# Optimization experiments

Measured on AMD Instinct MI355X. Metric: run time of the kernel, lower is better.

## Reference

```python
import jax, jax.numpy as jnp
import numpy as np

# init_kwargs constants
MIN_T = 0.01
MAX_T = 0.5
TGT_MIN = 0.005
TGT_MAX = 0.03
W_MIN = 15.0
W_MAX = 5.0
W_CONT = 5.0
W_SIZE = 7.0
LESION_T = 0.3


def setup_inputs() -> dict:
    key = jax.random.key(0)
    pred = jax.random.uniform(key, (16, 1, 128, 128, 128), dtype=jnp.float32)
    return {"pred": pred}


def reference(pred):
    # pred: [B, 1, D, H, W]
    s = pred[:, 0]  # [B, D, H, W]
    B = s.shape[0]
    axes = (1, 2, 3)

    # -- min/max activation penalties (per-sample threshold means) --
    act = jnp.mean((s > MIN_T).astype(s.dtype), axis=axes)          # [B]
    loss = jax.nn.relu(TGT_MIN - act) * W_MIN
    high = jnp.mean((s > MAX_T).astype(s.dtype), axis=axes)
    loss = loss + jax.nn.relu(high - TGT_MAX) * W_MAX

    # -- continuity penalty: mean abs finite differences along D,H,W --
    d_grad = jnp.mean(jnp.abs(s[:, 1:] - s[:, :-1]), axis=axes)
    h_grad = jnp.mean(jnp.abs(s[:, :, 1:] - s[:, :, :-1]), axis=axes)
    w_grad = jnp.mean(jnp.abs(s[:, :, :, 1:] - s[:, :, :, :-1]), axis=axes)
    avg_grad = (d_grad + h_grad + w_grad) / 3.0
    has_lesion = jnp.any(s > LESION_T, axis=axes)
    loss = loss + jnp.where(has_lesion, jnp.minimum(avg_grad, 1.0), 0.0) * W_CONT

    # -- size-variance penalty over masked active values (unbiased std, torch.std) --
    mask = (s > MIN_T).astype(s.dtype)
    cnt = jnp.sum(mask, axis=axes)                                   # [B]
    cnt_safe = jnp.maximum(cnt, 1.0)
    m = jnp.sum(s * mask, axis=axes) / cnt_safe                      # masked mean [B]
    sq = jnp.sum(mask * (s - m[:, None, None, None]) ** 2, axis=axes)
    gate = (act > 0.001) & (cnt > 1.0)
    var = jnp.where(gate, sq / jnp.maximum(cnt - 1.0, 1.0), 1.0)     # guard sqrt/grad when gated off
    std = jnp.sqrt(var)
    rel_std = std / (m + 1e-6)
    pen = jnp.exp(-5.0 * rel_std)
    loss = loss + jnp.where(gate, pen, 0.0) * W_SIZE

    return jnp.sum(loss) / B
```

## Files before the change

kernel.cpp:

```cpp
#include <hip/hip_runtime.h>
#include <math.h>

#define MIN_T    0.01f
#define MAX_T    0.5f
#define LESION_T 0.3f

constexpr int NB       = 16;
constexpr int DIM      = 128;
constexpr int PLANE_F4 = DIM * DIM / 4;
constexpr int VOX      = DIM * DIM * DIM;
constexpr int THREADS  = 256;
constexpr int HWBLKS   = PLANE_F4 / THREADS;
constexpr int DSEGS    = 4;
constexpr int DPS      = DIM / DSEGS;
constexpr int NACC     = 8;

__global__ __launch_bounds__(THREADS)
void partial_kernel(const float* __restrict__ pred, double* __restrict__ acc)
{
    const int seg   = blockIdx.x;
    const int hwblk = blockIdx.y;
    const int b     = blockIdx.z;
    const int tid   = (int)threadIdx.x;

    const float4* __restrict__ s4 =
        reinterpret_cast<const float4*>(pred + (size_t)b * VOX);

    const int  h    = hwblk * 8 + (tid >> 5);
    const bool do_h = (h < DIM - 1);
    const bool do_w = ((tid & 31) != 31);

    const int d0    = seg * DPS;
    const int d_end = (seg == DSEGS - 1) ? (DIM - 1) : (d0 + DPS);

    float cnt_min = 0.f, cnt_max = 0.f, sum_d = 0.f, sum_h = 0.f,
          sum_w = 0.f, sm = 0.f, sm2 = 0.f, les = 0.f;

    auto process = [&](const float4& v, const float4& vh) {
        const float xs[4] = { v.x, v.y, v.z, v.w };
        #pragma unroll
        for (int j = 0; j < 4; ++j) {
            const float x  = xs[j];
            const float mk = (x > MIN_T) ? 1.0f : 0.0f;
            cnt_min += mk;
            cnt_max += (x > MAX_T)    ? 1.0f : 0.0f;
            les     += (x > LESION_T) ? 1.0f : 0.0f;
            sm      += x * mk;
            sm2     += x * x * mk;
        }
        sum_w += fabsf(v.y - v.x) + fabsf(v.z - v.y) + fabsf(v.w - v.z);
        const float nx = __shfl_down(v.x, 1, 64);
        if (do_w) sum_w += fabsf(nx - v.w);
        if (do_h) sum_h += fabsf(vh.x - v.x) + fabsf(vh.y - v.y)
                         + fabsf(vh.z - v.z) + fabsf(vh.w - v.w);
    };

    const float4 zero4 = { 0.f, 0.f, 0.f, 0.f };
    size_t base = (size_t)d0 * PLANE_F4 + hwblk * THREADS + tid;
    float4 v  = s4[base];
    float4 vh = do_h ? s4[base + 32] : zero4;

    for (int d = d0 + 1; d <= d_end; ++d) {
        base += PLANE_F4;
        const float4 nv  = s4[base];
        const float4 nvh = do_h ? s4[base + 32] : zero4;
        process(v, vh);
        sum_d += fabsf(nv.x - v.x) + fabsf(nv.y - v.y)
               + fabsf(nv.z - v.z) + fabsf(nv.w - v.w);
        v = nv; vh = nvh;
    }
    if (seg == DSEGS - 1)
        process(v, vh);

    float vals[NACC] = { cnt_min, cnt_max, sum_d, sum_h, sum_w, sm, sm2, les };
    #pragma unroll
    for (int vi = 0; vi < NACC; ++vi) {
        float x = vals[vi];
        #pragma unroll
        for (int off = 32; off > 0; off >>= 1)
            x += __shfl_down(x, off, 64);
        vals[vi] = x;
    }

    __shared__ float smem[4][NACC];
    const int wave = tid >> 6;
    const int lane = tid & 63;
    if (lane == 0) {
        #pragma unroll
        for (int vi = 0; vi < NACC; ++vi) smem[wave][vi] = vals[vi];
    }
    __syncthreads();
    if (tid < NACC) {
        const float t = smem[0][tid] + smem[1][tid] +
                        smem[2][tid] + smem[3][tid];
        atomicAdd(&acc[(size_t)b * NACC + tid], (double)t);
    }
}

__global__ __launch_bounds__(64)
void finalize_kernel(const double* __restrict__ acc, float* __restrict__ out)
{
    float l = 0.0f;
    if (threadIdx.x < NB) {
        const double* a = acc + (size_t)threadIdx.x * NACC;
        const double cnt    = a[0];
        const double cntmax = a[1];
        const double sd     = a[2];
        const double sh     = a[3];
        const double sw     = a[4];
        const double sm     = a[5];
        const double sm2    = a[6];
        const double les    = a[7];

        const double inv_vox = 1.0 / (double)VOX;
        const double act  = cnt    * inv_vox;
        const double high = cntmax * inv_vox;

        double loss = fmax(0.005 - act, 0.0) * 15.0
                    + fmax(high - 0.03, 0.0) * 5.0;

        const double grad_den = 127.0 * 128.0 * 128.0;
        const double avg_grad = (sd + sh + sw) / (3.0 * grad_den);
        if (les > 0.5)
            loss += fmin(avg_grad, 1.0) * 5.0;

        const double cnt_safe = fmax(cnt, 1.0);
        const double m  = sm / cnt_safe;
        double sq = sm2 - 2.0 * m * sm + m * m * cnt;
        if (sq < 0.0) sq = 0.0;

        const bool gate = (act > 0.001) && (cnt > 1.0);
        if (gate) {
            const double var     = sq / fmax(cnt - 1.0, 1.0);
            const double rel_std = sqrt(var) / (m + 1e-6);
            loss += exp(-5.0 * rel_std) * 7.0;
        }
        l = (float)loss;
    }
    #pragma unroll
    for (int off = 32; off > 0; off >>= 1)
        l += __shfl_down(l, off, 64);
    if (threadIdx.x == 0)
        out[0] = l / (float)NB;
}

extern "C" void kernel_launch(void* const* d_in, const int* in_sizes, int n_in,
                              void* d_out, int out_size, void* d_ws, size_t ws_size,
                              hipStream_t stream)
{
    const float* pred = (const float*)d_in[0];
    float* out        = (float*)d_out;
    double* acc       = (double*)d_ws;

    hipMemsetAsync(d_ws, 0, (size_t)NB * NACC * sizeof(double), stream);

    dim3 grid(DSEGS, HWBLKS, NB);
    partial_kernel<<<grid, THREADS, 0, stream>>>(pred, acc);
    finalize_kernel<<<1, 64, 0, stream>>>(acc, out);
}
```

Before: 193.4 us.

## Share H-neighbor rows via LDS and replace double atomics with per-block slots

Blocks grow to 512 threads covering 16 rows, and each plane is staged in double-buffered shared memory so the H-neighbor value comes from LDS instead of a second global load. Only the last row of each block still fetches its boundary neighbor from global memory. Per-block partial sums go to distinct workspace slots instead of double-precision atomics, and the memset is dropped. The finalize kernel now reduces the 32 slots per sample. This adds a __syncthreads per depth step and doubles block size, which may reduce latency hiding.

```diff
diff --git a/kernel.cpp b/kernel.cpp
--- a/kernel.cpp
+++ b/kernel.cpp
@@ -9,32 +9,40 @@
 constexpr int DIM      = 128;
 constexpr int PLANE_F4 = DIM * DIM / 4;
 constexpr int VOX      = DIM * DIM * DIM;
-constexpr int THREADS  = 256;
-constexpr int HWBLKS   = PLANE_F4 / THREADS;
+constexpr int THREADS  = 512;
+constexpr int ROWS     = 16;
+constexpr int HWBLKS   = DIM / ROWS;
 constexpr int DSEGS    = 4;
 constexpr int DPS      = DIM / DSEGS;
 constexpr int NACC     = 8;
+constexpr int SLOTS_PER_B = DSEGS * HWBLKS;
+constexpr int NWAVES   = THREADS / 64;
 
 __global__ __launch_bounds__(THREADS)
-void partial_kernel(const float* __restrict__ pred, double* __restrict__ acc)
+void partial_kernel(const float* __restrict__ pred, float* __restrict__ ws)
 {
     const int seg   = blockIdx.x;
     const int hwblk = blockIdx.y;
     const int b     = blockIdx.z;
     const int tid   = (int)threadIdx.x;
+    const int r     = tid >> 5;
+    const bool last_row = (r == ROWS - 1);
+    const bool do_bnd = last_row && (hwblk < HWBLKS - 1);
+    const bool do_h   = !(last_row && hwblk == HWBLKS - 1);
+    const bool do_w   = ((tid & 31) != 31);
+
+    __shared__ float4 xbuf[2][THREADS];
+    __shared__ float  red[NWAVES][NACC];
 
     const float4* __restrict__ s4 =
         reinterpret_cast<const float4*>(pred + (size_t)b * VOX);
-
-    const int  h    = hwblk * 8 + (tid >> 5);
-    const bool do_h = (h < DIM - 1);
-    const bool do_w = ((tid & 31) != 31);
 
     const int d0    = seg * DPS;
     const int d_end = (seg == DSEGS - 1) ? (DIM - 1) : (d0 + DPS);
 
     float cnt_min = 0.f, cnt_max = 0.f, sum_d = 0.f, sum_h = 0.f,
           sum_w = 0.f, sm = 0.f, sm2 = 0.f, les = 0.f;
+    const float4 zero4 = { 0.f, 0.f, 0.f, 0.f };
 
     auto process = [&](const float4& v, const float4& vh) {
         const float xs[4] = { v.x, v.y, v.z, v.w };
@@ -55,19 +63,29 @@
                          + fabsf(vh.z - v.z) + fabsf(vh.w - v.w);
     };
 
-    const float4 zero4 = { 0.f, 0.f, 0.f, 0.f };
     size_t base = (size_t)d0 * PLANE_F4 + hwblk * THREADS + tid;
-    float4 v  = s4[base];
-    float4 vh = do_h ? s4[base + 32] : zero4;
+
+    float4 v   = s4[base];
+    float4 bvh = do_bnd ? s4[base + 32] : zero4;
+    int buf = 0;
+    xbuf[0][tid] = v;
+    __syncthreads();
+    float4 vh = !last_row ? xbuf[0][tid + 32] : bvh;
 
     for (int d = d0 + 1; d <= d_end; ++d) {
         base += PLANE_F4;
-        const float4 nv  = s4[base];
-        const float4 nvh = do_h ? s4[base + 32] : zero4;
+        const float4 nv   = s4[base];
+        const float4 nbvh = do_bnd ? s4[base + 32] : zero4;
+        xbuf[buf ^ 1][tid] = nv;
+
         process(v, vh);
         sum_d += fabsf(nv.x - v.x) + fabsf(nv.y - v.y)
                + fabsf(nv.z - v.z) + fabsf(nv.w - v.w);
-        v = nv; vh = nvh;
+
+        __syncthreads();
+        vh = !last_row ? xbuf[buf ^ 1][tid + 32] : nbvh;
+        v = nv;
+        buf ^= 1;
     }
     if (seg == DSEGS - 1)
         process(v, vh);
@@ -82,27 +100,43 @@
         vals[vi] = x;
     }
 
-    __shared__ float smem[4][NACC];
     const int wave = tid >> 6;
     const int lane = tid & 63;
     if (lane == 0) {
         #pragma unroll
-        for (int vi = 0; vi < NACC; ++vi) smem[wave][vi] = vals[vi];
+        for (int vi = 0; vi < NACC; ++vi) red[wave][vi] = vals[vi];
     }
     __syncthreads();
     if (tid < NACC) {
-        const float t = smem[0][tid] + smem[1][tid] +
-                        smem[2][tid] + smem[3][tid];
-        atomicAdd(&acc[(size_t)b * NACC + tid], (double)t);
+        float t = 0.f;
+        #pragma unroll
+        for (int w = 0; w < NWAVES; ++w) t += red[w][tid];
+        const int slot = b * SLOTS_PER_B + hwblk * DSEGS + seg;
+        ws[(size_t)slot * NACC + tid] = t;
     }
 }
 
-__global__ __launch_bounds__(64)
-void finalize_kernel(const double* __restrict__ acc, float* __restrict__ out)
+__global__ __launch_bounds__(512)
+void finalize_kernel(const float* __restrict__ ws, float* __restrict__ out)
 {
-    float l = 0.0f;
-    if (threadIdx.x < NB) {
-        const double* a = acc + (size_t)threadIdx.x * NACC;
+    const int tid = (int)threadIdx.x;
+    const int b   = tid >> 5;
+    const int k   = tid & 31;
+
+    double a[NACC];
+    const float* p = ws + ((size_t)(b * SLOTS_PER_B + k)) * NACC;
+    #pragma unroll
+    for (int vi = 0; vi < NACC; ++vi) a[vi] = (double)p[vi];
+
+    #pragma unroll
+    for (int vi = 0; vi < NACC; ++vi) {
+        #pragma unroll
+        for (int off = 16; off > 0; off >>= 1)
+            a[vi] += __shfl_down(a[vi], off, 32);
+    }
+
+    __shared__ double bl[NB];
+    if (k == 0) {
         const double cnt    = a[0];
         const double cntmax = a[1];
         const double sd     = a[2];
@@ -135,13 +169,15 @@
             const double rel_std = sqrt(var) / (m + 1e-6);
             loss += exp(-5.0 * rel_std) * 7.0;
         }
-        l = (float)loss;
+        bl[b] = loss;
     }
-    #pragma unroll
-    for (int off = 32; off > 0; off >>= 1)
-        l += __shfl_down(l, off, 64);
-    if (threadIdx.x == 0)
-        out[0] = l / (float)NB;
+    __syncthreads();
+    if (tid == 0) {
+        double s = 0.0;
+        #pragma unroll
+        for (int i = 0; i < NB; ++i) s += bl[i];
+        out[0] = (float)(s / (double)NB);
+    }
 }
 
 extern "C" void kernel_launch(void* const* d_in, const int* in_sizes, int n_in,
@@ -150,11 +186,9 @@
 {
     const float* pred = (const float*)d_in[0];
     float* out        = (float*)d_out;
-    double* acc       = (double*)d_ws;
-
-    hipMemsetAsync(d_ws, 0, (size_t)NB * NACC * sizeof(double), stream);
+    float* ws         = (float*)d_ws;
 
     dim3 grid(DSEGS, HWBLKS, NB);
-    partial_kernel<<<grid, THREADS, 0, stream>>>(pred, acc);
-    finalize_kernel<<<1, 64, 0, stream>>>(acc, out);
+    partial_kernel<<<grid, THREADS, 0, stream>>>(pred, ws);
+    finalize_kernel<<<1, 512, 0, stream>>>(ws, out);
 }
```

Measured after the change: 194.6 us. No clear change (+0.7%).
